# Kernel optimization log

Measured on AMD Instinct MI355X. Metric: run time of the kernel, lower is better.

Reference implementation:

```python
import jax, jax.numpy as jnp
import numpy as np

HID, HEADS, FFN = 2048, 16, 8192
HEAD_DIM = HID // HEADS
B, S = 2, 2048
EPS = 1e-5


def setup_inputs() -> dict:
    key = jax.random.key(0)
    ks = jax.random.split(key, 12)
    s = 0.02
    x = jax.random.normal(ks[0], (B, S, HID), dtype=jnp.float32)
    # additive causal mask: 0 on/below diagonal, -inf-like above
    neg = jnp.float32(-1e9)
    causal = jnp.where(jnp.tril(jnp.ones((S, S), dtype=bool)), 0.0, neg)
    mask = causal[None, None, :, :].astype(jnp.float32)
    return {
        "x": x,
        "mask": mask,
        "ln1_w": jnp.ones((HID,), jnp.float32),
        "ln1_b": jnp.zeros((HID,), jnp.float32),
        "q_w": jax.random.normal(ks[1], (HID, HID), jnp.float32) * s,
        "k_w": jax.random.normal(ks[2], (HID, HID), jnp.float32) * s,
        "v_w": jax.random.normal(ks[3], (HID, HID), jnp.float32) * s,
        "o_w": jax.random.normal(ks[4], (HID, HID), jnp.float32) * s,
        "ln2_w": jnp.ones((HID,), jnp.float32),
        "ln2_b": jnp.zeros((HID,), jnp.float32),
        "w1_w": jax.random.normal(ks[5], (FFN, HID), jnp.float32) * s,
        "w1_b": jnp.zeros((FFN,), jnp.float32),
        "wg_w": jax.random.normal(ks[6], (FFN, HID), jnp.float32) * s,
        "w2_w": jax.random.normal(ks[7], (HID, FFN), jnp.float32) * s,
        "w2_b": jnp.zeros((HID,), jnp.float32),
    }


def _layernorm(x, w, b):
    mu = jnp.mean(x, axis=-1, keepdims=True)
    var = jnp.mean(jnp.square(x - mu), axis=-1, keepdims=True)
    return (x - mu) * jax.lax.rsqrt(var + EPS) * w + b


def reference(x, mask, ln1_w, ln1_b, q_w, k_w, v_w, o_w,
              ln2_w, ln2_b, w1_w, w1_b, wg_w, w2_w, w2_b):
    b, s, _ = x.shape
    # --- attention sublayer ---
    h = _layernorm(x, ln1_w, ln1_b)
    def split_heads(y):  # [b,s,hid] -> [b,H,s,d]
        return y.reshape(b, s, HEADS, HEAD_DIM).transpose(0, 2, 1, 3)
    q = split_heads(h @ q_w.T)
    k = split_heads(h @ k_w.T)
    v = split_heads(h @ v_w.T)
    scale = jnp.sqrt(jnp.float32(HEAD_DIM))
    scores = jnp.einsum('bhqd,bhkd->bhqk', q, k) / scale + mask
    weights = jax.nn.softmax(scores, axis=-1)
    attn = jnp.einsum('bhqk,bhkd->bhqd', weights, v)
    attn = attn.transpose(0, 2, 1, 3).reshape(b, s, HID)
    x = x + attn @ o_w.T
    # --- SwiGLU FFN sublayer ---
    h2 = _layernorm(x, ln2_w, ln2_b)
    ff = jax.nn.silu(h2 @ w1_w.T + w1_b) * (h2 @ wg_w.T)
    x = x + ff @ w2_w.T + w2_b
    return x
```

## Files before the change

### kernel.cpp

```cpp
#include <hip/hip_runtime.h>
#include <cstdint>
#include <cstddef>

#define HIDN 2048
#define NROWS 4096
#define FFND 8192
#define SEQ 2048
#define QKVN 6144

typedef __attribute__((ext_vector_type(8))) __bf16 bf16x8;
typedef __attribute__((ext_vector_type(4))) float f32x4;

__device__ __forceinline__ unsigned short f2b(float f) {
    union { float f; unsigned u; } v; v.f = f;
    unsigned r = v.u + 0x7fffu + ((v.u >> 16) & 1u);
    return (unsigned short)(r >> 16);
}
__device__ __forceinline__ float b2f(unsigned short h) {
    union { unsigned u; float f; } v; v.u = ((unsigned)h) << 16; return v.f;
}
__device__ __forceinline__ void gload16(const void* g, void* lds) {
    __builtin_amdgcn_global_load_lds(
        (const __attribute__((address_space(1))) void*)g,
        (__attribute__((address_space(3))) void*)lds, 16, 0, 0);
}

__global__ __launch_bounds__(256) void f2b_kernel(const float* __restrict__ in,
                                                  unsigned short* __restrict__ out, int n4) {
    int i = blockIdx.x * 256 + threadIdx.x;
    if (i < n4) {
        float4 v = ((const float4*)in)[i];
        ushort4 o;
        o.x = f2b(v.x); o.y = f2b(v.y); o.z = f2b(v.z); o.w = f2b(v.w);
        ((ushort4*)out)[i] = o;
    }
}

__global__ __launch_bounds__(256) void ln_kernel(const float* __restrict__ x,
                                                 const float* __restrict__ w,
                                                 const float* __restrict__ b,
                                                 unsigned short* __restrict__ out) {
    int row = blockIdx.x, tid = threadIdx.x;
    const float4* xr = (const float4*)(x + (size_t)row * HIDN);
    float4 a0 = xr[tid], a1 = xr[tid + 256];
    float s  = a0.x + a0.y + a0.z + a0.w + a1.x + a1.y + a1.z + a1.w;
    float s2 = a0.x*a0.x + a0.y*a0.y + a0.z*a0.z + a0.w*a0.w
             + a1.x*a1.x + a1.y*a1.y + a1.z*a1.z + a1.w*a1.w;
#pragma unroll
    for (int i = 1; i < 64; i <<= 1) { s += __shfl_xor(s, i); s2 += __shfl_xor(s2, i); }
    __shared__ float red[8];
    if ((tid & 63) == 0) { red[tid >> 6] = s; red[4 + (tid >> 6)] = s2; }
    __syncthreads();
    s  = red[0] + red[1] + red[2] + red[3];
    s2 = red[4] + red[5] + red[6] + red[7];
    float mu  = s * (1.0f / HIDN);
    float var = s2 * (1.0f / HIDN) - mu * mu;
    float rstd = rsqrtf(var + 1e-5f);
    const float4* wv = (const float4*)w;
    const float4* bv = (const float4*)b;
    float4 w0 = wv[tid], w1 = wv[tid + 256], b0 = bv[tid], b1 = bv[tid + 256];
    ushort4 o0, o1;
    o0.x = f2b((a0.x - mu) * rstd * w0.x + b0.x);
    o0.y = f2b((a0.y - mu) * rstd * w0.y + b0.y);
    o0.z = f2b((a0.z - mu) * rstd * w0.z + b0.z);
    o0.w = f2b((a0.w - mu) * rstd * w0.w + b0.w);
    o1.x = f2b((a1.x - mu) * rstd * w1.x + b1.x);
    o1.y = f2b((a1.y - mu) * rstd * w1.y + b1.y);
    o1.z = f2b((a1.z - mu) * rstd * w1.z + b1.z);
    o1.w = f2b((a1.w - mu) * rstd * w1.w + b1.w);
    ushort4* orow = (ushort4*)(out + (size_t)row * HIDN);
    orow[tid] = o0; orow[tid + 256] = o1;
}

template <int EPI>
__global__ __launch_bounds__(256)
void gemm_bt(const unsigned short* __restrict__ A, const unsigned short* __restrict__ Bw,
             int M, int N, int K, int tiles_n, float scale,
             const float* __restrict__ bias, const float* __restrict__ resf,
             const unsigned short* __restrict__ aux,
             float* __restrict__ outf, unsigned short* __restrict__ outb) {
    __shared__ unsigned short Asm[2][128 * 32];
    __shared__ unsigned short Bsm[2][128 * 32];
    int tid = threadIdx.x;
    int wave = tid >> 6, lane = tid & 63;
    int lrow = lane & 15, quad = lane >> 4;
    int bm = blockIdx.x / tiles_n, bn = blockIdx.x % tiles_n;
    int wm = (wave >> 1) * 64, wn = (wave & 1) * 64;

    f32x4 acc[4][4];
#pragma unroll
    for (int i = 0; i < 4; i++)
#pragma unroll
        for (int j = 0; j < 4; j++) acc[i][j] = f32x4{0.f, 0.f, 0.f, 0.f};

    int srow = wave * 32 + (lane >> 2);
    int scol = (lane & 3) * 8;
    const unsigned short* Ag = A + (size_t)(bm * 128 + srow) * K + scol;
    const unsigned short* Bg = Bw + (size_t)(bn * 128 + srow) * K + scol;

    for (int k0 = 0; k0 < K; k0 += 64) {
#pragma unroll
        for (int s = 0; s < 2; s++) {
            gload16(Ag + k0 + s * 32, &Asm[s][(wave * 2 + 0) * 512]);
            gload16(Ag + k0 + s * 32 + (size_t)16 * K, &Asm[s][(wave * 2 + 1) * 512]);
            gload16(Bg + k0 + s * 32, &Bsm[s][(wave * 2 + 0) * 512]);
            gload16(Bg + k0 + s * 32 + (size_t)16 * K, &Bsm[s][(wave * 2 + 1) * 512]);
        }
        __syncthreads();
#pragma unroll
        for (int s = 0; s < 2; s++) {
            bf16x8 af[4], bfb[4];
#pragma unroll
            for (int mi = 0; mi < 4; mi++)
                af[mi] = *(const bf16x8*)&Asm[s][(wm + mi * 16 + lrow) * 32 + quad * 8];
#pragma unroll
            for (int ni = 0; ni < 4; ni++)
                bfb[ni] = *(const bf16x8*)&Bsm[s][(wn + ni * 16 + lrow) * 32 + quad * 8];
#pragma unroll
            for (int mi = 0; mi < 4; mi++)
#pragma unroll
                for (int ni = 0; ni < 4; ni++)
                    acc[mi][ni] = __builtin_amdgcn_mfma_f32_16x16x32_bf16(af[mi], bfb[ni], acc[mi][ni], 0, 0, 0);
        }
        __syncthreads();
    }

    int row0 = bm * 128 + wm, col0 = bn * 128 + wn;
#pragma unroll
    for (int mi = 0; mi < 4; mi++) {
#pragma unroll
        for (int ni = 0; ni < 4; ni++) {
            int c = col0 + ni * 16 + lrow;
#pragma unroll
            for (int r = 0; r < 4; r++) {
                int rr = row0 + mi * 16 + quad * 4 + r;
                size_t idx = (size_t)rr * N + c;
                float vv = acc[mi][ni][r];
                if constexpr (EPI == 0) {
                    outb[idx] = f2b(vv * scale);
                } else if constexpr (EPI == 1) {
                    outf[idx] = vv + resf[idx];
                } else if constexpr (EPI == 2) {
                    outb[idx] = f2b(vv + bias[c]);
                } else if constexpr (EPI == 3) {
                    float av = b2f(aux[idx]);
                    float sl = av / (1.f + __expf(-av));
                    outb[idx] = f2b(sl * vv);
                } else if constexpr (EPI == 4) {
                    outf[idx] = vv + bias[c] + resf[idx];
                } else if constexpr (EPI == 5) {
                    outb[idx] = f2b(vv * (c < HIDN ? scale : 1.0f));
                }
            }
        }
    }
}

__global__ __launch_bounds__(256)
void attn_kernel(const unsigned short* __restrict__ qkv, unsigned short* __restrict__ o) {
    int bh = blockIdx.x;
    int qt = 31 - blockIdx.y;
    int b = bh >> 4, h = bh & 15;
    int tid = threadIdx.x, wave = tid >> 6, lane = tid & 63;
    int lrow = lane & 15, quad = lane >> 4;
    int q0 = qt * 64;
    size_t base = ((size_t)b * SEQ) * QKVN + h * 128;
    const unsigned short* qp0 = qkv + base;
    const unsigned short* kp0 = qkv + base + HIDN;
    const unsigned short* vp0 = qkv + base + 2 * HIDN;
    size_t obase = ((size_t)b * SEQ) * HIDN + h * 128;

    __shared__ unsigned short Ksm[64 * 136];
    __shared__ unsigned short VTsm[128 * 72];
    __shared__ unsigned short Psm[4 * 16 * 72];

    bf16x8 qf[4];
    {
        const unsigned short* qp = qp0 + (size_t)(q0 + wave * 16 + lrow) * QKVN + quad * 8;
#pragma unroll
        for (int kc = 0; kc < 4; kc++) qf[kc] = *(const bf16x8*)(qp + kc * 32);
    }

    f32x4 oacc[8];
#pragma unroll
    for (int i = 0; i < 8; i++) oacc[i] = f32x4{0.f, 0.f, 0.f, 0.f};
    float m_run[4], l_run[4];
    int rowg[4];
#pragma unroll
    for (int r = 0; r < 4; r++) {
        m_run[r] = -1e30f; l_run[r] = 0.f;
        rowg[r] = q0 + wave * 16 + quad * 4 + r;
    }

    for (int kt = 0; kt <= qt; ++kt) {
        {
            int r = tid >> 2, cc = (tid & 3) * 32;
            const uint4* src = (const uint4*)(kp0 + (size_t)(kt * 64 + r) * QKVN + cc);
            uint4* dst = (uint4*)&Ksm[r * 136 + cc];
            dst[0] = src[0]; dst[1] = src[1]; dst[2] = src[2]; dst[3] = src[3];
        }
        {
            int kv = (tid >> 3) * 2, d0 = (tid & 7) * 16;
            const unsigned short* vp = vp0 + (size_t)(kt * 64 + kv) * QKVN + d0;
            unsigned short va[16], vb[16];
            *(uint4*)&va[0] = ((const uint4*)vp)[0];
            *(uint4*)&va[8] = ((const uint4*)vp)[1];
            *(uint4*)&vb[0] = ((const uint4*)(vp + QKVN))[0];
            *(uint4*)&vb[8] = ((const uint4*)(vp + QKVN))[1];
#pragma unroll
            for (int i = 0; i < 16; i++) {
                unsigned pair = (unsigned)va[i] | ((unsigned)vb[i] << 16);
                *(unsigned*)&VTsm[(d0 + i) * 72 + kv] = pair;
            }
        }
        __syncthreads();

        f32x4 sacc[4];
#pragma unroll
        for (int ns = 0; ns < 4; ns++) sacc[ns] = f32x4{0.f, 0.f, 0.f, 0.f};
#pragma unroll
        for (int ns = 0; ns < 4; ns++) {
            const unsigned short* kb = &Ksm[(ns * 16 + lrow) * 136 + quad * 8];
#pragma unroll
            for (int kc = 0; kc < 4; kc++) {
                bf16x8 kf = *(const bf16x8*)(kb + kc * 32);
                sacc[ns] = __builtin_amdgcn_mfma_f32_16x16x32_bf16(qf[kc], kf, sacc[ns], 0, 0, 0);
            }
        }
#pragma unroll
        for (int ns = 0; ns < 4; ns++) {
            int colg = kt * 64 + ns * 16 + lrow;
#pragma unroll
            for (int r = 0; r < 4; r++)
                if (colg > rowg[r]) sacc[ns][r] = -1e30f;
        }
        float mnew[4], alpha[4], rsum[4];
#pragma unroll
        for (int r = 0; r < 4; r++) {
            float mv = fmaxf(fmaxf(sacc[0][r], sacc[1][r]), fmaxf(sacc[2][r], sacc[3][r]));
#pragma unroll
            for (int off = 1; off < 16; off <<= 1) mv = fmaxf(mv, __shfl_xor(mv, off));
            mnew[r] = fmaxf(m_run[r], mv);
            alpha[r] = __expf(m_run[r] - mnew[r]);
            rsum[r] = 0.f;
        }
#pragma unroll
        for (int ns = 0; ns < 4; ns++)
#pragma unroll
            for (int r = 0; r < 4; r++) {
                float p = __expf(sacc[ns][r] - mnew[r]);
                sacc[ns][r] = p;
                rsum[r] += p;
            }
#pragma unroll
        for (int r = 0; r < 4; r++) {
#pragma unroll
            for (int off = 1; off < 16; off <<= 1) rsum[r] += __shfl_xor(rsum[r], off);
            l_run[r] = l_run[r] * alpha[r] + rsum[r];
            m_run[r] = mnew[r];
        }
#pragma unroll
        for (int nc = 0; nc < 8; nc++)
#pragma unroll
            for (int r = 0; r < 4; r++) oacc[nc][r] *= alpha[r];

        unsigned short* pw = &Psm[wave * 16 * 72];
#pragma unroll
        for (int ns = 0; ns < 4; ns++)
#pragma unroll
            for (int r = 0; r < 4; r++)
                pw[(quad * 4 + r) * 72 + ns * 16 + lrow] = f2b(sacc[ns][r]);
        __syncthreads();
        bf16x8 pf[2];
#pragma unroll
        for (int kc = 0; kc < 2; kc++)
            pf[kc] = *(const bf16x8*)&pw[lrow * 72 + kc * 32 + quad * 8];
#pragma unroll
        for (int nc = 0; nc < 8; nc++) {
#pragma unroll
            for (int kc = 0; kc < 2; kc++) {
                bf16x8 vf = *(const bf16x8*)&VTsm[(nc * 16 + lrow) * 72 + kc * 32 + quad * 8];
                oacc[nc] = __builtin_amdgcn_mfma_f32_16x16x32_bf16(pf[kc], vf, oacc[nc], 0, 0, 0);
            }
        }
        __syncthreads();
    }

    float inv[4];
#pragma unroll
    for (int r = 0; r < 4; r++) inv[r] = 1.f / l_run[r];
#pragma unroll
    for (int nc = 0; nc < 8; nc++) {
#pragma unroll
        for (int r = 0; r < 4; r++) {
            int srow = q0 + wave * 16 + quad * 4 + r;
            o[obase + (size_t)srow * HIDN + nc * 16 + lrow] = f2b(oacc[nc][r] * inv[r]);
        }
    }
}

extern "C" void kernel_launch(void* const* d_in, const int* in_sizes, int n_in,
                              void* d_out, int out_size, void* d_ws, size_t ws_size,
                              hipStream_t stream) {
    const float* x    = (const float*)d_in[0];
    const float* ln1w = (const float*)d_in[2];
    const float* ln1b = (const float*)d_in[3];
    const float* qw   = (const float*)d_in[4];
    const float* kw   = (const float*)d_in[5];
    const float* vw   = (const float*)d_in[6];
    const float* ow   = (const float*)d_in[7];
    const float* ln2w = (const float*)d_in[8];
    const float* ln2b = (const float*)d_in[9];
    const float* w1w  = (const float*)d_in[10];
    const float* w1bias = (const float*)d_in[11];
    const float* wgw  = (const float*)d_in[12];
    const float* w2w  = (const float*)d_in[13];
    const float* w2bias = (const float*)d_in[14];
    float* out = (float*)d_out;

    char* ws = (char*)d_ws;
    const size_t MB = 1ull << 20;
    unsigned short* qkvwb = (unsigned short*)(ws + 0 * MB);
    unsigned short* owb  = (unsigned short*)(ws + 24 * MB);
    unsigned short* w1wb = (unsigned short*)(ws + 32 * MB);
    unsigned short* wgwb = (unsigned short*)(ws + 64 * MB);
    unsigned short* w2wb = (unsigned short*)(ws + 96 * MB);
    unsigned short* a1   = (unsigned short*)(ws + 128 * MB);
    unsigned short* hbuf = (unsigned short*)(ws + 128 * MB);
    unsigned short* qkvb = (unsigned short*)(ws + 144 * MB);
    unsigned short* attnb= (unsigned short*)(ws + 192 * MB);
    unsigned short* h2   = (unsigned short*)(ws + 208 * MB);
    float*          x1   = out;

    f2b_kernel<<<4096, 256, 0, stream>>>(qw, qkvwb, HIDN * HIDN / 4);
    f2b_kernel<<<4096, 256, 0, stream>>>(kw, qkvwb + (size_t)HIDN * HIDN, HIDN * HIDN / 4);
    f2b_kernel<<<4096, 256, 0, stream>>>(vw, qkvwb + (size_t)2 * HIDN * HIDN, HIDN * HIDN / 4);
    f2b_kernel<<<4096, 256, 0, stream>>>(ow, owb, HIDN * HIDN / 4);
    f2b_kernel<<<16384, 256, 0, stream>>>(w1w, w1wb, FFND * HIDN / 4);
    f2b_kernel<<<16384, 256, 0, stream>>>(wgw, wgwb, FFND * HIDN / 4);
    f2b_kernel<<<16384, 256, 0, stream>>>(w2w, w2wb, HIDN * FFND / 4);

    ln_kernel<<<NROWS, 256, 0, stream>>>(x, ln1w, ln1b, hbuf);

    const float qscale = 0.08838834764831845f;
    gemm_bt<5><<<dim3(32 * 48), 256, 0, stream>>>(hbuf, qkvwb, NROWS, QKVN, HIDN, 48, qscale,
                                                  nullptr, nullptr, nullptr, nullptr, qkvb);
    attn_kernel<<<dim3(32, 32), 256, 0, stream>>>(qkvb, attnb);
    gemm_bt<1><<<dim3(32 * 16), 256, 0, stream>>>(attnb, owb, NROWS, HIDN, HIDN, 16, 1.0f,
                                                  nullptr, x, nullptr, x1, nullptr);
    ln_kernel<<<NROWS, 256, 0, stream>>>(x1, ln2w, ln2b, h2);
    gemm_bt<2><<<dim3(32 * 64), 256, 0, stream>>>(h2, w1wb, NROWS, FFND, HIDN, 64, 1.0f,
                                                  w1bias, nullptr, nullptr, nullptr, a1);
    gemm_bt<3><<<dim3(32 * 64), 256, 0, stream>>>(h2, wgwb, NROWS, FFND, HIDN, 64, 1.0f,
                                                  nullptr, nullptr, a1, nullptr, a1);
    gemm_bt<4><<<dim3(32 * 16), 256, 0, stream>>>(a1, w2wb, NROWS, HIDN, FFND, 16, 1.0f,
                                                  w2bias, x1, nullptr, out, nullptr);
    (void)in_sizes; (void)n_in; (void)out_size; (void)ws_size;
}
```

Measured before the change: 1.191 ms.

## Double attention query tile per block and fuse weight conversions into one launch

The attention kernel now processes 128 query rows per block, two 16-row subtiles per wave, so each K/V tile loaded into shared memory is reused across twice as many queries. The per-wave P buffer handoff now uses an LDS waitcnt instead of a block barrier. The seven fp32-to-bf16 weight conversion launches are merged into one kernel that picks its source by index range. The trade-off is higher register pressure, fewer blocks (512) for the causal attention grid, and coarser diagonal-tile masking waste.

```diff
diff --git a/kernel.cpp b/kernel.cpp
--- a/kernel.cpp
+++ b/kernel.cpp
@@ -25,15 +25,25 @@
         (__attribute__((address_space(3))) void*)lds, 16, 0, 0);
 }
 
-__global__ __launch_bounds__(256) void f2b_kernel(const float* __restrict__ in,
-                                                  unsigned short* __restrict__ out, int n4) {
+__global__ __launch_bounds__(256) void convall_kernel(
+    const float* __restrict__ s0, const float* __restrict__ s1,
+    const float* __restrict__ s2, const float* __restrict__ s3,
+    const float* __restrict__ s4, const float* __restrict__ s5,
+    const float* __restrict__ s6, unsigned short* __restrict__ dst) {
+    const int M1 = 1 << 20;
     int i = blockIdx.x * 256 + threadIdx.x;
-    if (i < n4) {
-        float4 v = ((const float4*)in)[i];
-        ushort4 o;
-        o.x = f2b(v.x); o.y = f2b(v.y); o.z = f2b(v.z); o.w = f2b(v.w);
-        ((ushort4*)out)[i] = o;
-    }
+    const float* src; int rel;
+    if      (i <  1 * M1) { src = s0; rel = i;          }
+    else if (i <  2 * M1) { src = s1; rel = i - 1 * M1; }
+    else if (i <  3 * M1) { src = s2; rel = i - 2 * M1; }
+    else if (i <  4 * M1) { src = s3; rel = i - 3 * M1; }
+    else if (i <  8 * M1) { src = s4; rel = i - 4 * M1; }
+    else if (i < 12 * M1) { src = s5; rel = i - 8 * M1; }
+    else                  { src = s6; rel = i - 12 * M1; }
+    float4 v = ((const float4*)src)[rel];
+    ushort4 o;
+    o.x = f2b(v.x); o.y = f2b(v.y); o.z = f2b(v.z); o.w = f2b(v.w);
+    ((ushort4*)dst)[i] = o;
 }
 
 __global__ __launch_bounds__(256) void ln_kernel(const float* __restrict__ x,
@@ -159,11 +169,11 @@
 __global__ __launch_bounds__(256)
 void attn_kernel(const unsigned short* __restrict__ qkv, unsigned short* __restrict__ o) {
     int bh = blockIdx.x;
-    int qt = 31 - blockIdx.y;
+    int qt = 15 - blockIdx.y;
     int b = bh >> 4, h = bh & 15;
     int tid = threadIdx.x, wave = tid >> 6, lane = tid & 63;
     int lrow = lane & 15, quad = lane >> 4;
-    int q0 = qt * 64;
+    int q0 = qt * 128;
     size_t base = ((size_t)b * SEQ) * QKVN + h * 128;
     const unsigned short* qp0 = qkv + base;
     const unsigned short* kp0 = qkv + base + HIDN;
@@ -172,27 +182,33 @@
 
     __shared__ unsigned short Ksm[64 * 136];
     __shared__ unsigned short VTsm[128 * 72];
-    __shared__ unsigned short Psm[4 * 16 * 72];
-
-    bf16x8 qf[4];
-    {
-        const unsigned short* qp = qp0 + (size_t)(q0 + wave * 16 + lrow) * QKVN + quad * 8;
-#pragma unroll
-        for (int kc = 0; kc < 4; kc++) qf[kc] = *(const bf16x8*)(qp + kc * 32);
-    }
-
-    f32x4 oacc[8];
-#pragma unroll
-    for (int i = 0; i < 8; i++) oacc[i] = f32x4{0.f, 0.f, 0.f, 0.f};
-    float m_run[4], l_run[4];
-    int rowg[4];
-#pragma unroll
-    for (int r = 0; r < 4; r++) {
-        m_run[r] = -1e30f; l_run[r] = 0.f;
-        rowg[r] = q0 + wave * 16 + quad * 4 + r;
-    }
-
-    for (int kt = 0; kt <= qt; ++kt) {
+    __shared__ unsigned short Psm[4 * 32 * 72];
+
+    bf16x8 qf[2][4];
+#pragma unroll
+    for (int mt = 0; mt < 2; mt++) {
+        const unsigned short* qp = qp0 + (size_t)(q0 + wave * 32 + mt * 16 + lrow) * QKVN + quad * 8;
+#pragma unroll
+        for (int kc = 0; kc < 4; kc++) qf[mt][kc] = *(const bf16x8*)(qp + kc * 32);
+    }
+
+    f32x4 oacc[2][8];
+#pragma unroll
+    for (int mt = 0; mt < 2; mt++)
+#pragma unroll
+        for (int i = 0; i < 8; i++) oacc[mt][i] = f32x4{0.f, 0.f, 0.f, 0.f};
+    float m_run[2][4], l_run[2][4];
+    int rowg[2][4];
+#pragma unroll
+    for (int mt = 0; mt < 2; mt++)
+#pragma unroll
+        for (int r = 0; r < 4; r++) {
+            m_run[mt][r] = -1e30f; l_run[mt][r] = 0.f;
+            rowg[mt][r] = q0 + wave * 32 + mt * 16 + quad * 4 + r;
+        }
+
+    int kt_max = 2 * qt + 1;
+    for (int kt = 0; kt <= kt_max; ++kt) {
         {
             int r = tid >> 2, cc = (tid & 3) * 32;
             const uint4* src = (const uint4*)(kp0 + (size_t)(kt * 64 + r) * QKVN + cc);
@@ -215,87 +231,102 @@
         }
         __syncthreads();
 
-        f32x4 sacc[4];
-#pragma unroll
-        for (int ns = 0; ns < 4; ns++) sacc[ns] = f32x4{0.f, 0.f, 0.f, 0.f};
+        f32x4 sacc[2][4];
+#pragma unroll
+        for (int mt = 0; mt < 2; mt++)
+#pragma unroll
+            for (int ns = 0; ns < 4; ns++) sacc[mt][ns] = f32x4{0.f, 0.f, 0.f, 0.f};
 #pragma unroll
         for (int ns = 0; ns < 4; ns++) {
             const unsigned short* kb = &Ksm[(ns * 16 + lrow) * 136 + quad * 8];
 #pragma unroll
             for (int kc = 0; kc < 4; kc++) {
                 bf16x8 kf = *(const bf16x8*)(kb + kc * 32);
-                sacc[ns] = __builtin_amdgcn_mfma_f32_16x16x32_bf16(qf[kc], kf, sacc[ns], 0, 0, 0);
-            }
-        }
-#pragma unroll
-        for (int ns = 0; ns < 4; ns++) {
-            int colg = kt * 64 + ns * 16 + lrow;
-#pragma unroll
-            for (int r = 0; r < 4; r++)
-                if (colg > rowg[r]) sacc[ns][r] = -1e30f;
-        }
-        float mnew[4], alpha[4], rsum[4];
-#pragma unroll
-        for (int r = 0; r < 4; r++) {
-            float mv = fmaxf(fmaxf(sacc[0][r], sacc[1][r]), fmaxf(sacc[2][r], sacc[3][r]));
-#pragma unroll
-            for (int off = 1; off < 16; off <<= 1) mv = fmaxf(mv, __shfl_xor(mv, off));
-            mnew[r] = fmaxf(m_run[r], mv);
-            alpha[r] = __expf(m_run[r] - mnew[r]);
-            rsum[r] = 0.f;
-        }
-#pragma unroll
-        for (int ns = 0; ns < 4; ns++)
+#pragma unroll
+                for (int mt = 0; mt < 2; mt++)
+                    sacc[mt][ns] = __builtin_amdgcn_mfma_f32_16x16x32_bf16(qf[mt][kc], kf, sacc[mt][ns], 0, 0, 0);
+            }
+        }
+#pragma unroll
+        for (int mt = 0; mt < 2; mt++) {
+#pragma unroll
+            for (int ns = 0; ns < 4; ns++) {
+                int colg = kt * 64 + ns * 16 + lrow;
+#pragma unroll
+                for (int r = 0; r < 4; r++)
+                    if (colg > rowg[mt][r]) sacc[mt][ns][r] = -1e30f;
+            }
+            float mnew[4], alpha[4], rsum[4];
 #pragma unroll
             for (int r = 0; r < 4; r++) {
-                float p = __expf(sacc[ns][r] - mnew[r]);
-                sacc[ns][r] = p;
-                rsum[r] += p;
-            }
-#pragma unroll
-        for (int r = 0; r < 4; r++) {
-#pragma unroll
-            for (int off = 1; off < 16; off <<= 1) rsum[r] += __shfl_xor(rsum[r], off);
-            l_run[r] = l_run[r] * alpha[r] + rsum[r];
-            m_run[r] = mnew[r];
-        }
+                float mv = fmaxf(fmaxf(sacc[mt][0][r], sacc[mt][1][r]),
+                                 fmaxf(sacc[mt][2][r], sacc[mt][3][r]));
+#pragma unroll
+                for (int off = 1; off < 16; off <<= 1) mv = fmaxf(mv, __shfl_xor(mv, off));
+                mnew[r] = fmaxf(m_run[mt][r], mv);
+                alpha[r] = __expf(m_run[mt][r] - mnew[r]);
+                rsum[r] = 0.f;
+            }
+#pragma unroll
+            for (int ns = 0; ns < 4; ns++)
+#pragma unroll
+                for (int r = 0; r < 4; r++) {
+                    float p = __expf(sacc[mt][ns][r] - mnew[r]);
+                    sacc[mt][ns][r] = p;
+                    rsum[r] += p;
+                }
+#pragma unroll
+            for (int r = 0; r < 4; r++) {
+#pragma unroll
+                for (int off = 1; off < 16; off <<= 1) rsum[r] += __shfl_xor(rsum[r], off);
+                l_run[mt][r] = l_run[mt][r] * alpha[r] + rsum[r];
+                m_run[mt][r] = mnew[r];
+            }
+#pragma unroll
+            for (int nc = 0; nc < 8; nc++)
+#pragma unroll
+                for (int r = 0; r < 4; r++) oacc[mt][nc][r] *= alpha[r];
+        }
+
+        unsigned short* pw = &Psm[wave * 32 * 72];
+#pragma unroll
+        for (int mt = 0; mt < 2; mt++)
+#pragma unroll
+            for (int ns = 0; ns < 4; ns++)
+#pragma unroll
+                for (int r = 0; r < 4; r++)
+                    pw[(mt * 16 + quad * 4 + r) * 72 + ns * 16 + lrow] = f2b(sacc[mt][ns][r]);
+        asm volatile("s_waitcnt lgkmcnt(0)" ::: "memory");
+        bf16x8 pf[2][2];
+#pragma unroll
+        for (int mt = 0; mt < 2; mt++)
+#pragma unroll
+            for (int kc = 0; kc < 2; kc++)
+                pf[mt][kc] = *(const bf16x8*)&pw[(mt * 16 + lrow) * 72 + kc * 32 + quad * 8];
 #pragma unroll
         for (int nc = 0; nc < 8; nc++)
-#pragma unroll
-            for (int r = 0; r < 4; r++) oacc[nc][r] *= alpha[r];
-
-        unsigned short* pw = &Psm[wave * 16 * 72];
-#pragma unroll
-        for (int ns = 0; ns < 4; ns++)
-#pragma unroll
-            for (int r = 0; r < 4; r++)
-                pw[(quad * 4 + r) * 72 + ns * 16 + lrow] = f2b(sacc[ns][r]);
-        __syncthreads();
-        bf16x8 pf[2];
-#pragma unroll
-        for (int kc = 0; kc < 2; kc++)
-            pf[kc] = *(const bf16x8*)&pw[lrow * 72 + kc * 32 + quad * 8];
-#pragma unroll
-        for (int nc = 0; nc < 8; nc++) {
 #pragma unroll
             for (int kc = 0; kc < 2; kc++) {
                 bf16x8 vf = *(const bf16x8*)&VTsm[(nc * 16 + lrow) * 72 + kc * 32 + quad * 8];
-                oacc[nc] = __builtin_amdgcn_mfma_f32_16x16x32_bf16(pf[kc], vf, oacc[nc], 0, 0, 0);
-            }
-        }
+#pragma unroll
+                for (int mt = 0; mt < 2; mt++)
+                    oacc[mt][nc] = __builtin_amdgcn_mfma_f32_16x16x32_bf16(pf[mt][kc], vf, oacc[mt][nc], 0, 0, 0);
+            }
         __syncthreads();
     }
 
-    float inv[4];
-#pragma unroll
-    for (int r = 0; r < 4; r++) inv[r] = 1.f / l_run[r];
-#pragma unroll
-    for (int nc = 0; nc < 8; nc++) {
-#pragma unroll
-        for (int r = 0; r < 4; r++) {
-            int srow = q0 + wave * 16 + quad * 4 + r;
-            o[obase + (size_t)srow * HIDN + nc * 16 + lrow] = f2b(oacc[nc][r] * inv[r]);
-        }
+#pragma unroll
+    for (int mt = 0; mt < 2; mt++) {
+        float inv[4];
+#pragma unroll
+        for (int r = 0; r < 4; r++) inv[r] = 1.f / l_run[mt][r];
+#pragma unroll
+        for (int nc = 0; nc < 8; nc++)
+#pragma unroll
+            for (int r = 0; r < 4; r++) {
+                int srow = q0 + wave * 32 + mt * 16 + quad * 4 + r;
+                o[obase + (size_t)srow * HIDN + nc * 16 + lrow] = f2b(oacc[mt][nc][r] * inv[r]);
+            }
     }
 }
 
@@ -320,6 +351,7 @@
 
     char* ws = (char*)d_ws;
     const size_t MB = 1ull << 20;
+    unsigned short* wall  = (unsigned short*)(ws + 0 * MB);
     unsigned short* qkvwb = (unsigned short*)(ws + 0 * MB);
     unsigned short* owb  = (unsigned short*)(ws + 24 * MB);
     unsigned short* w1wb = (unsigned short*)(ws + 32 * MB);
@@ -332,20 +364,14 @@
     unsigned short* h2   = (unsigned short*)(ws + 208 * MB);
     float*          x1   = out;
 
-    f2b_kernel<<<4096, 256, 0, stream>>>(qw, qkvwb, HIDN * HIDN / 4);
-    f2b_kernel<<<4096, 256, 0, stream>>>(kw, qkvwb + (size_t)HIDN * HIDN, HIDN * HIDN / 4);
-    f2b_kernel<<<4096, 256, 0, stream>>>(vw, qkvwb + (size_t)2 * HIDN * HIDN, HIDN * HIDN / 4);
-    f2b_kernel<<<4096, 256, 0, stream>>>(ow, owb, HIDN * HIDN / 4);
-    f2b_kernel<<<16384, 256, 0, stream>>>(w1w, w1wb, FFND * HIDN / 4);
-    f2b_kernel<<<16384, 256, 0, stream>>>(wgw, wgwb, FFND * HIDN / 4);
-    f2b_kernel<<<16384, 256, 0, stream>>>(w2w, w2wb, HIDN * FFND / 4);
+    convall_kernel<<<65536, 256, 0, stream>>>(qw, kw, vw, ow, w1w, wgw, w2w, wall);
 
     ln_kernel<<<NROWS, 256, 0, stream>>>(x, ln1w, ln1b, hbuf);
 
     const float qscale = 0.08838834764831845f;
     gemm_bt<5><<<dim3(32 * 48), 256, 0, stream>>>(hbuf, qkvwb, NROWS, QKVN, HIDN, 48, qscale,
                                                   nullptr, nullptr, nullptr, nullptr, qkvb);
-    attn_kernel<<<dim3(32, 32), 256, 0, stream>>>(qkvb, attnb);
+    attn_kernel<<<dim3(32, 16), 256, 0, stream>>>(qkvb, attnb);
     gemm_bt<1><<<dim3(32 * 16), 256, 0, stream>>>(attnb, owb, NROWS, HIDN, HIDN, 16, 1.0f,
                                                   nullptr, x, nullptr, x1, nullptr);
     ln_kernel<<<NROWS, 256, 0, stream>>>(x1, ln2w, ln2b, h2);
```

Result: no change. 1.202 ms (+0.9%).
